# Optimization experiments

Measured on AMD Instinct MI355X. Metric: run time of the kernel, lower is better.

## Reference

```python
import jax, jax.numpy as jnp
import numpy as np

B, S, D, H = 4, 2048, 1024, 16
HD = D // H  # head_dim = 64


def setup_inputs() -> dict:
    key = jax.random.key(0)
    ks = jax.random.split(key, 6)
    scale = 0.02
    x = jax.random.normal(ks[0], (B, S, D), dtype=jnp.float32)
    # per-head projection weights, torch Linear is y = x @ W.T; store as [H, D, HD]
    Wq = jax.random.normal(ks[1], (H, D, HD), dtype=jnp.float32) * scale
    Wk = jax.random.normal(ks[2], (H, D, HD), dtype=jnp.float32) * scale
    Wv = jax.random.normal(ks[3], (H, D, HD), dtype=jnp.float32) * scale
    Wo = jax.random.normal(ks[4], (D, D), dtype=jnp.float32) * scale  # torch [out, in]
    bo = jax.random.normal(ks[5], (D,), dtype=jnp.float32) * scale
    return {"x": x, "Wq": Wq, "Wk": Wk, "Wv": Wv, "Wo": Wo, "bo": bo}


def reference(x, Wq, Wk, Wv, Wo, bo):
    # project: [B,S,D] x [H,D,HD] -> [B,H,S,HD]
    q = jnp.einsum("bsd,hde->bhse", x, Wq)
    k = jnp.einsum("bsd,hde->bhse", x, Wk)
    v = jnp.einsum("bsd,hde->bhse", x, Wv)
    scores = jnp.einsum("bhse,bhte->bhst", q, k) / jnp.sqrt(jnp.float32(HD))
    causal = jnp.tril(jnp.ones((S, S), dtype=bool))  # same as registered tril mask
    scores = jnp.where(causal, scores, -jnp.inf)
    w = jax.nn.softmax(scores, axis=-1)
    out = jnp.einsum("bhst,bhte->bhse", w, v)  # [B,H,S,HD]
    # concat heads along feature dim: [B,S,H*HD] = [B,S,D]
    out = out.transpose(0, 2, 1, 3).reshape(B, S, D)
    # output projection: torch Linear y = x @ W.T + b
    return jnp.einsum("bsd,od->bso", out, Wo) + bo
```

## Files before the change

### kernel.cpp

```cpp
#include <hip/hip_runtime.h>
#include <hip/hip_bf16.h>

typedef __bf16 bf16x8 __attribute__((ext_vector_type(8)));
typedef float f32x4 __attribute__((ext_vector_type(4)));
typedef unsigned short u16x4 __attribute__((ext_vector_type(4)));
typedef unsigned short u16x8 __attribute__((ext_vector_type(8)));
typedef unsigned uint4v __attribute__((ext_vector_type(4)));

#define B_ 4
#define S_ 2048
#define D_ 1024
#define H_ 16
#define HD_ 64

__device__ __forceinline__ unsigned short f2bf(float f) {
  unsigned u = __float_as_uint(f);
  u += 0x7fff + ((u >> 16) & 1);
  return (unsigned short)(u >> 16);
}

__device__ __forceinline__ void gload16(const void* g, void* l) {
  __builtin_amdgcn_global_load_lds((const __attribute__((address_space(1))) unsigned int*)g,
                                   (__attribute__((address_space(3))) unsigned int*)l,
                                   16, 0, 0);
}

__global__ void pack_x_k(const float* __restrict__ in, unsigned short* __restrict__ out, int n4) {
  int i = blockIdx.x * blockDim.x + threadIdx.x;
  int stride = gridDim.x * blockDim.x;
  for (; i < n4; i += stride) {
    float4 v = reinterpret_cast<const float4*>(in)[i];
    u16x4 o = {f2bf(v.x), f2bf(v.y), f2bf(v.z), f2bf(v.w)};
    reinterpret_cast<u16x4*>(out)[i] = o;
  }
}

__global__ void pack_wqkv_k(const float* __restrict__ Wq, const float* __restrict__ Wk,
                            const float* __restrict__ Wv, unsigned short* __restrict__ Wt) {
  int o = blockIdx.x * blockDim.x + threadIdx.x;
  int n = o >> 10;
  int d = o & 1023;
  const float* W = (n < 1024) ? Wq : (n < 2048) ? Wk : Wv;
  int nn = n & 1023;
  int h = nn >> 6, e = nn & 63;
  Wt[o] = f2bf(W[(h << 16) + (d << 6) + e]);
}

template <int ADD_BIAS>
__global__ __launch_bounds__(256, 2) void gemm_bt_k(const unsigned short* __restrict__ A,
                                                    const unsigned short* __restrict__ Bt,
                                                    void* __restrict__ C,
                                                    const float* __restrict__ bias,
                                                    int M, int N, int K) {
  __shared__ __align__(16) unsigned short lA[2][128 * 64];
  __shared__ __align__(16) unsigned short lB[2][128 * 64];
  const int tid = threadIdx.x;
  const int wid = tid >> 6, lane = tid & 63;
  const int r = lane & 15, g = lane >> 4;
  const long arow0 = (long)blockIdx.x * 128;
  const long brow0 = (long)blockIdx.y * 128;
  const int wr = (wid >> 1) * 64, wc = (wid & 1) * 64;

  const f32x4 z4 = {0.f, 0.f, 0.f, 0.f};
  f32x4 acc[4][4];
#pragma unroll
  for (int m = 0; m < 4; ++m)
#pragma unroll
    for (int n = 0; n < 4; ++n) acc[m][n] = z4;

  auto stage = [&](int buf, int k0) {
#pragma unroll
    for (int c = 0; c < 4; ++c) {
      const int j = c * 256 + wid * 64 + lane;
      const int row = j >> 3, col = (j & 7) * 8;
      gload16(A + (arow0 + row) * K + k0 + col, &lA[buf][(c * 256 + wid * 64) * 8]);
      gload16(Bt + (brow0 + row) * K + k0 + col, &lB[buf][(c * 256 + wid * 64) * 8]);
    }
  };

  stage(0, 0);
  __syncthreads();
  const int nk = K >> 6;
  for (int kt = 0; kt < nk; ++kt) {
    const int cur = kt & 1;
    if (kt + 1 < nk) stage(cur ^ 1, (kt + 1) << 6);
#pragma unroll
    for (int kk = 0; kk < 2; ++kk) {
      bf16x8 af[4], bfr[4];
#pragma unroll
      for (int m = 0; m < 4; ++m)
        af[m] = *(const bf16x8*)&lA[cur][(wr + m * 16 + r) * 64 + kk * 32 + g * 8];
#pragma unroll
      for (int n = 0; n < 4; ++n)
        bfr[n] = *(const bf16x8*)&lB[cur][(wc + n * 16 + r) * 64 + kk * 32 + g * 8];
#pragma unroll
      for (int m = 0; m < 4; ++m)
#pragma unroll
        for (int n = 0; n < 4; ++n)
          acc[m][n] = __builtin_amdgcn_mfma_f32_16x16x32_bf16(af[m], bfr[n], acc[m][n], 0, 0, 0);
    }
    __syncthreads();
  }

#pragma unroll
  for (int m = 0; m < 4; ++m) {
#pragma unroll
    for (int n = 0; n < 4; ++n) {
#pragma unroll
      for (int rr = 0; rr < 4; ++rr) {
        const long row = arow0 + wr + m * 16 + g * 4 + rr;
        const long col = brow0 + wc + n * 16 + r;
        const float v = acc[m][n][rr];
        if (ADD_BIAS) {
          ((float*)C)[row * N + col] = v + bias[col];
        } else {
          ((unsigned short*)C)[row * N + col] = f2bf(v);
        }
      }
    }
  }
}

__global__ __launch_bounds__(256, 2) void attn_k(const unsigned short* __restrict__ qkv,
                                                 unsigned short* __restrict__ out) {
  __shared__ __align__(16) unsigned short lK[2][64 * 64];
  __shared__ __align__(16) unsigned short lVt[2][64 * 64];

  const int tid = threadIdx.x, wid = tid >> 6, lane = tid & 63;
  const int r = lane & 15, g = lane >> 4;
  const int bh = blockIdx.x;
  const int b = bh >> 4, h = bh & 15;
  const int qb = 15 - (int)blockIdx.y;
  const int q0 = qb * 128;

  const long base = ((long)b * S_) * 3072 + h * 64;
  const unsigned short* Qg = qkv + base;
  const unsigned short* Kg = qkv + base + 1024;
  const unsigned short* Vg = qkv + base + 2048;

  int qrow[2];
  bf16x8 qf[2][2];
#pragma unroll
  for (int qs = 0; qs < 2; ++qs) {
    qrow[qs] = q0 + qs * 64 + wid * 16 + r;
#pragma unroll
    for (int kk = 0; kk < 2; ++kk)
      qf[qs][kk] = *(const bf16x8*)&Qg[(long)qrow[qs] * 3072 + kk * 32 + g * 8];
  }

  const f32x4 z4 = {0.f, 0.f, 0.f, 0.f};
  f32x4 o[2][4];
#pragma unroll
  for (int qs = 0; qs < 2; ++qs)
#pragma unroll
    for (int nt = 0; nt < 4; ++nt) o[qs][nt] = z4;
  float m_i[2] = {-1e30f, -1e30f};
  float l_i[2] = {0.f, 0.f};

  u16x8 kreg[2], vreg[2];
  auto load_regs = [&](int t0) {
#pragma unroll
    for (int c = 0; c < 2; ++c) {
      const int j = c * 256 + tid;
      const int tt = j >> 3, e0 = (j & 7) * 8;
      kreg[c] = *(const u16x8*)&Kg[(long)(t0 + tt) * 3072 + e0];
      const int tc = j & 63, ec = j >> 6;
      vreg[c] = *(const u16x8*)&Vg[(long)(t0 + tc) * 3072 + ec * 8];
    }
  };
  auto write_lds = [&](int buf) {
#pragma unroll
    for (int c = 0; c < 2; ++c) {
      const int j = c * 256 + tid;
      const int row = j >> 3, cc = j & 7;
      *(u16x8*)&lK[buf][(row * 8 + (cc ^ (row & 7))) * 8] = kreg[c];
      const int tc = j & 63, ec = j >> 6;
#pragma unroll
      for (int i = 0; i < 8; ++i) {
        const int e = ec * 8 + i;
        lVt[buf][e * 64 + (tc ^ (i * 8))] = vreg[c][i];
      }
    }
  };

  const int ntiles = (q0 >> 6) + 2;
  load_regs(0);
  write_lds(0);

  for (int t = 0; t < ntiles; ++t) {
    const int cur = t & 1;
    if (t + 1 < ntiles) load_regs((t + 1) << 6);
    __syncthreads();

    const int t0 = t << 6;
    const bool act0 = (t < ntiles - 1);
    const bool diag0 = (t == ntiles - 2);
    const bool diag1 = (t == ntiles - 1);

    f32x4 st[2][4];
#pragma unroll
    for (int tt = 0; tt < 4; ++tt) { st[0][tt] = z4; st[1][tt] = z4; }
    __builtin_amdgcn_s_setprio(1);
#pragma unroll
    for (int kk = 0; kk < 2; ++kk)
#pragma unroll
      for (int tt = 0; tt < 4; ++tt) {
        const int row = tt * 16 + r, cc = kk * 4 + g;
        bf16x8 kf = *(const bf16x8*)&lK[cur][(row * 8 + (cc ^ (row & 7))) * 8];
        st[1][tt] = __builtin_amdgcn_mfma_f32_16x16x32_bf16(kf, qf[1][kk], st[1][tt], 0, 0, 0);
        if (act0)
          st[0][tt] = __builtin_amdgcn_mfma_f32_16x16x32_bf16(kf, qf[0][kk], st[0][tt], 0, 0, 0);
      }
    __builtin_amdgcn_s_setprio(0);

    bf16x8 pf[2][2];
    unsigned corr_bits[2] = {0x3f800000u, 0x3f800000u};
    bool dodef[2] = {true, true};
#pragma unroll
    for (int qs = 0; qs < 2; ++qs) {
      if (qs == 0 && !act0) continue;
      const bool diag = qs ? diag1 : diag0;
      float sv[16];
#pragma unroll
      for (int tt = 0; tt < 4; ++tt)
#pragma unroll
        for (int rg = 0; rg < 4; ++rg) {
          float s = st[qs][tt][rg] * 0.125f;
          if (diag && (t0 + tt * 16 + g * 4 + rg > qrow[qs])) s = -1e30f;
          sv[tt * 4 + rg] = s;
        }
      float h0 = fmaxf(fmaxf(fmaxf(sv[0], sv[1]), fmaxf(sv[2], sv[3])),
                       fmaxf(fmaxf(sv[4], sv[5]), fmaxf(sv[6], sv[7])));
      float h1 = fmaxf(fmaxf(fmaxf(sv[8], sv[9]), fmaxf(sv[10], sv[11])),
                       fmaxf(fmaxf(sv[12], sv[13]), fmaxf(sv[14], sv[15])));
      const float pmax = fmaxf(h0, h1);
      const bool defer = __all(pmax - m_i[qs] <= 8.f);
      float corr = 1.f;
      if (!defer) {
        float mx = fmaxf(pmax, m_i[qs]);
        mx = fmaxf(mx, __shfl_xor(mx, 16, 64));
        mx = fmaxf(mx, __shfl_xor(mx, 32, 64));
        corr = __expf(m_i[qs] - mx);
        m_i[qs] = mx;
      }
      dodef[qs] = defer;
      corr_bits[qs] = __float_as_uint(corr);
      float p[16];
      float rs = 0.f;
#pragma unroll
      for (int i = 0; i < 16; ++i) {
        p[i] = __expf(sv[i] - m_i[qs]);
        rs += p[i];
      }
      rs += __shfl_xor(rs, 16, 64);
      rs += __shfl_xor(rs, 32, 64);
      l_i[qs] = l_i[qs] * corr + rs;
      unsigned cw[4][2];
#pragma unroll
      for (int tt = 0; tt < 4; ++tt)
#pragma unroll
        for (int e = 0; e < 2; ++e)
          asm("v_cvt_pk_bf16_f32 %0, %1, %2"
              : "=v"(cw[tt][e]) : "v"(p[tt * 4 + 2 * e]), "v"(p[tt * 4 + 2 * e + 1]));
#pragma unroll
      for (int kk = 0; kk < 2; ++kk) {
        unsigned x0 = cw[2 * kk][0], y0 = cw[2 * kk + 1][0];
        unsigned x1 = cw[2 * kk][1], y1 = cw[2 * kk + 1][1];
        asm volatile("v_permlane32_swap_b32 %0, %1" : "+v"(x0), "+v"(y0));
        asm volatile("v_permlane16_swap_b32 %0, %1" : "+v"(x0), "+v"(y0));
        asm volatile("v_permlane32_swap_b32 %0, %1" : "+v"(x1), "+v"(y1));
        asm volatile("v_permlane16_swap_b32 %0, %1" : "+v"(x1), "+v"(y1));
        uint4v w = {x0, x1, y0, y1};
        pf[qs][kk] = *(bf16x8*)&w;
      }
    }
#pragma unroll
    for (int qs = 0; qs < 2; ++qs) {
      if (qs == 0 && !act0) continue;
      if (!dodef[qs]) {
        const float corr = __uint_as_float(corr_bits[qs]);
#pragma unroll
        for (int rr = 0; rr < 4; ++rr) {
          const float c = __shfl(corr, g * 4 + rr, 64);
#pragma unroll
          for (int nt = 0; nt < 4; ++nt) o[qs][nt][rr] *= c;
        }
      }
    }

    __builtin_amdgcn_s_setprio(1);
#pragma unroll
    for (int kk = 0; kk < 2; ++kk)
#pragma unroll
      for (int nt = 0; nt < 4; ++nt) {
        const int row = nt * 16 + r, cc = kk * 4 + g;
        const bf16x8 vf = *(const bf16x8*)&lVt[cur][(row * 8 + (cc ^ (row & 7))) * 8];
        o[1][nt] = __builtin_amdgcn_mfma_f32_16x16x32_bf16(pf[1][kk], vf, o[1][nt], 0, 0, 0);
        if (act0)
          o[0][nt] = __builtin_amdgcn_mfma_f32_16x16x32_bf16(pf[0][kk], vf, o[0][nt], 0, 0, 0);
      }
    __builtin_amdgcn_s_setprio(0);

    if (t + 1 < ntiles) write_lds(cur ^ 1);
  }

#pragma unroll
  for (int qs = 0; qs < 2; ++qs) {
    float linv[4];
#pragma unroll
    for (int rr = 0; rr < 4; ++rr)
      linv[rr] = 1.f / __shfl(l_i[qs], g * 4 + rr, 64);
#pragma unroll
    for (int nt = 0; nt < 4; ++nt)
#pragma unroll
      for (int rr = 0; rr < 4; ++rr) {
        const long s = q0 + qs * 64 + wid * 16 + g * 4 + rr;
        out[((long)b * S_ + s) * 1024 + h * 64 + nt * 16 + r] = f2bf(o[qs][nt][rr] * linv[rr]);
      }
  }
}

extern "C" void kernel_launch(void* const* d_in, const int* in_sizes, int n_in,
                              void* d_out, int out_size, void* d_ws, size_t ws_size,
                              hipStream_t stream) {
  const float* x = (const float*)d_in[0];
  const float* Wq = (const float*)d_in[1];
  const float* Wk = (const float*)d_in[2];
  const float* Wv = (const float*)d_in[3];
  const float* Wo = (const float*)d_in[4];
  const float* bo = (const float*)d_in[5];
  float* out = (float*)d_out;

  char* ws = (char*)d_ws;
  unsigned short* Xb = (unsigned short*)(ws);
  unsigned short* Wt = (unsigned short*)(ws + (16ul << 20));
  unsigned short* Wob = (unsigned short*)(ws + (22ul << 20));
  unsigned short* QKV = (unsigned short*)(ws + (24ul << 20));
  unsigned short* AO = (unsigned short*)(ws + (72ul << 20));

  pack_x_k<<<2048, 256, 0, stream>>>(x, Xb, (B_ * S_ * D_) / 4);
  pack_x_k<<<512, 256, 0, stream>>>(Wo, Wob, (D_ * D_) / 4);
  pack_wqkv_k<<<(3 * D_ * D_) / 256, 256, 0, stream>>>(Wq, Wk, Wv, Wt);

  gemm_bt_k<0><<<dim3(64, 24), 256, 0, stream>>>(Xb, Wt, QKV, nullptr, B_ * S_, 3 * D_, D_);
  attn_k<<<dim3(64, 16), 256, 0, stream>>>(QKV, AO);
  gemm_bt_k<1><<<dim3(64, 8), 256, 0, stream>>>(AO, Wob, out, bo, B_ * S_, D_, D_);
}
```

Before: 200.4 us.

## Add 256x256-tile QKV GEMM with swizzled LDS and phased prefetch

Replaces the QKV projection GEMM with a new 512-thread kernel that computes 256x256 output tiles. It uses XOR-swizzled LDS layout, a two-deep async global-to-LDS pipeline split into half-tile phases with manual waitcnt/barrier control, MFMA priority boosting, and an XCD-aware block remapping. The larger tile raises data reuse per LDS load and the phasing is meant to overlap loads with MFMA. In exchange it uses much more LDS (128KB) and more accumulator registers, which lowers occupancy, and the hand-counted vmcnt waits are fragile. The old templated GEMM is specialized to the bias/fp32 output path.

Measured after the change: 199.3 us. About the same (-0.6%).

```diff
diff --git a/kernel.cpp b/kernel.cpp
--- a/kernel.cpp
+++ b/kernel.cpp
@@ -46,10 +46,114 @@
   Wt[o] = f2bf(W[(h << 16) + (d << 6) + e]);
 }
 
-template <int ADD_BIAS>
+__global__ __launch_bounds__(512, 2) void gemm256_k(const unsigned short* __restrict__ A,
+                                                    const unsigned short* __restrict__ Bt,
+                                                    unsigned short* __restrict__ C,
+                                                    int M, int N, int K) {
+  __shared__ __align__(16) unsigned short lds[2][2][2][128 * 64];
+  const int tid = threadIdx.x;
+  const int wid = tid >> 6, lane = tid & 63;
+  const int r = lane & 15, g = lane >> 4;
+  const int wm = wid >> 2, wn = wid & 3;
+
+  int id = blockIdx.y * gridDim.x + blockIdx.x;
+  const int cpx = (gridDim.x * gridDim.y) >> 3;
+  id = (id & 7) * cpx + (id >> 3);
+  const long arow0 = (long)(id % gridDim.x) * 256;
+  const long bcol0 = (long)(id / gridDim.x) * 256;
+
+  const f32x4 z4 = {0.f, 0.f, 0.f, 0.f};
+  f32x4 acc[8][4];
+#pragma unroll
+  for (int m = 0; m < 8; ++m)
+#pragma unroll
+    for (int n = 0; n < 4; ++n) acc[m][n] = z4;
+
+  auto stage_half = [&](int kt, int op, int h) {
+    const unsigned short* src = op ? Bt + (bcol0 + 128 * h) * K : A + (arow0 + 128 * h) * K;
+    const int k0 = kt << 6;
+    unsigned short* base = &lds[kt & 1][op][h][0];
+#pragma unroll
+    for (int c = 0; c < 2; ++c) {
+      const int j = c * 512 + (wid << 6) + lane;
+      const int row = j >> 3, cc = j & 7;
+      const int ccs = cc ^ (row & 7);
+      gload16(src + (long)row * K + k0 + ccs * 8, base + (c * 512 + (wid << 6)) * 8);
+    }
+  };
+
+  const int nk = K >> 6;
+  stage_half(0, 0, 0);
+  stage_half(0, 1, 0);
+  stage_half(0, 0, 1);
+  stage_half(0, 1, 1);
+  stage_half(1, 0, 0);
+  stage_half(1, 1, 0);
+  asm volatile("s_waitcnt vmcnt(8)" ::: "memory");
+  asm volatile("s_barrier" ::: "memory");
+
+  for (int t = 0; t < nk; ++t) {
+    const int buf = t & 1;
+#pragma unroll
+    for (int ph = 0; ph < 4; ++ph) {
+      const int mh = ph >> 1, nh = ph & 1;
+      bf16x8 af[4][2], bfv[2][2];
+#pragma unroll
+      for (int i = 0; i < 4; ++i)
+#pragma unroll
+        for (int kk = 0; kk < 2; ++kk) {
+          const int rowh = (2 * i + wm) * 16 + r;
+          af[i][kk] = *(const bf16x8*)&lds[buf][0][mh][rowh * 64 + (((kk << 2) + g) ^ (rowh & 7)) * 8];
+        }
+#pragma unroll
+      for (int j = 0; j < 2; ++j)
+#pragma unroll
+        for (int kk = 0; kk < 2; ++kk) {
+          const int rowh = (4 * j + wn) * 16 + r;
+          bfv[j][kk] = *(const bf16x8*)&lds[buf][1][nh][rowh * 64 + (((kk << 2) + g) ^ (rowh & 7)) * 8];
+        }
+      if (ph == 0) { if (t + 1 < nk) stage_half(t + 1, 0, 1); }
+      if (ph == 1) { if (t + 1 < nk) stage_half(t + 1, 1, 1); }
+      if (ph == 2) { if (t + 2 < nk) stage_half(t + 2, 0, 0); }
+      if (ph == 3) { if (t + 2 < nk) stage_half(t + 2, 1, 0); }
+      asm volatile("s_barrier" ::: "memory");
+      __builtin_amdgcn_s_setprio(1);
+#pragma unroll
+      for (int kk = 0; kk < 2; ++kk)
+#pragma unroll
+        for (int i = 0; i < 4; ++i)
+#pragma unroll
+          for (int j = 0; j < 2; ++j)
+            acc[4 * mh + i][2 * nh + j] = __builtin_amdgcn_mfma_f32_16x16x32_bf16(
+                af[i][kk], bfv[j][kk], acc[4 * mh + i][2 * nh + j], 0, 0, 0);
+      __builtin_amdgcn_s_setprio(0);
+      if (ph == 0) {
+        if (t + 1 < nk) asm volatile("s_waitcnt vmcnt(6)" ::: "memory");
+        else            asm volatile("s_waitcnt vmcnt(0)" ::: "memory");
+      }
+      if (ph == 3) {
+        if (t + 2 < nk)      asm volatile("s_waitcnt vmcnt(8)" ::: "memory");
+        else if (t + 1 < nk) asm volatile("s_waitcnt vmcnt(4)" ::: "memory");
+      }
+      asm volatile("s_waitcnt lgkmcnt(0)\n\ts_barrier" ::: "memory");
+    }
+  }
+
+#pragma unroll
+  for (int m = 0; m < 8; ++m)
+#pragma unroll
+    for (int n = 0; n < 4; ++n)
+#pragma unroll
+      for (int rr = 0; rr < 4; ++rr) {
+        const long row = arow0 + (2 * m + wm) * 16 + g * 4 + rr;
+        const long col = bcol0 + (4 * n + wn) * 16 + r;
+        C[row * N + col] = f2bf(acc[m][n][rr]);
+      }
+}
+
 __global__ __launch_bounds__(256, 2) void gemm_bt_k(const unsigned short* __restrict__ A,
                                                     const unsigned short* __restrict__ Bt,
-                                                    void* __restrict__ C,
+                                                    float* __restrict__ C,
                                                     const float* __restrict__ bias,
                                                     int M, int N, int K) {
   __shared__ __align__(16) unsigned short lA[2][128 * 64];
@@ -110,12 +214,7 @@
       for (int rr = 0; rr < 4; ++rr) {
         const long row = arow0 + wr + m * 16 + g * 4 + rr;
         const long col = brow0 + wc + n * 16 + r;
-        const float v = acc[m][n][rr];
-        if (ADD_BIAS) {
-          ((float*)C)[row * N + col] = v + bias[col];
-        } else {
-          ((unsigned short*)C)[row * N + col] = f2bf(v);
-        }
+        C[row * N + col] = acc[m][n][rr] + bias[col];
       }
     }
   }
@@ -342,7 +441,7 @@
   pack_x_k<<<512, 256, 0, stream>>>(Wo, Wob, (D_ * D_) / 4);
   pack_wqkv_k<<<(3 * D_ * D_) / 256, 256, 0, stream>>>(Wq, Wk, Wv, Wt);
 
-  gemm_bt_k<0><<<dim3(64, 24), 256, 0, stream>>>(Xb, Wt, QKV, nullptr, B_ * S_, 3 * D_, D_);
+  gemm256_k<<<dim3(32, 12), 512, 0, stream>>>(Xb, Wt, QKV, B_ * S_, 3 * D_, D_);
   attn_k<<<dim3(64, 16), 256, 0, stream>>>(QKV, AO);
-  gemm_bt_k<1><<<dim3(64, 8), 256, 0, stream>>>(AO, Wob, out, bo, B_ * S_, D_, D_);
-}
+  gemm_bt_k<<<dim3(64, 8), 256, 0, stream>>>(AO, Wob, out, bo, B_ * S_, D_, D_);
+}
```
